# Kernel optimization log

Hardware: AMD Instinct MI355X
Metric: run time of the kernel (lower is better)

The kernel has to match this reference:

```python
import jax, jax.numpy as jnp
import numpy as np

N_DST = 25000
LEAKY = 0.2
EPS = 1e-5


def _params(dim_node=128, dim_edge=128, dim_time=100, dim_out=128):
    ks = jax.random.split(jax.random.key(1), 8)
    dq = dim_node + dim_time
    dk = dim_node + dim_edge + dim_time
    do = dim_node + dim_out
    p = {
        'w_t': jnp.asarray((1.0 / 10 ** np.linspace(0, 9, dim_time, dtype=np.float32)).reshape(dim_time, 1)),
        'b_t': jnp.zeros((dim_time,), jnp.float32),
        'Wq': jax.random.normal(ks[0], (dim_out, dq), jnp.float32) * (dq ** -0.5),
        'bq': jnp.zeros((dim_out,), jnp.float32),
        'Wk': jax.random.normal(ks[1], (dim_out, dk), jnp.float32) * (dk ** -0.5),
        'bk': jnp.zeros((dim_out,), jnp.float32),
        'Wv': jax.random.normal(ks[2], (dim_out, dk), jnp.float32) * (dk ** -0.5),
        'bv': jnp.zeros((dim_out,), jnp.float32),
        'Wout': jax.random.normal(ks[3], (dim_out, do), jnp.float32) * (do ** -0.5),
        'bout': jnp.zeros((dim_out,), jnp.float32),
        'ln_w': jnp.ones((dim_out,), jnp.float32),
        'ln_b': jnp.zeros((dim_out,), jnp.float32),
    }
    return p


def setup_inputs() -> dict:
    key = jax.random.key(0)
    k1, k2, k3, k4, k5 = jax.random.split(key, 5)
    E = 400000
    inp = {
        'h': jax.random.normal(k1, (425000, 128), jnp.float32),
        'f': jax.random.normal(k2, (E, 128), jnp.float32),
        'dt': jax.random.uniform(k3, (E,), jnp.float32) * 1e4,
        'src_idx': jax.random.randint(k4, (E,), 0, 425000, jnp.int32),
        'dst_idx': jax.random.randint(k5, (E,), 0, N_DST, jnp.int32),
    }
    inp.update(_params())
    return inp


def reference(h, f, dt, src_idx, dst_idx, w_t, b_t, Wq, bq, Wk, bk, Wv, bv, Wout, bout, ln_w, ln_b):
    num_head = 2
    dim_out = Wq.shape[0]
    E = dt.shape[0]
    # time encoding: cos(Linear(t))
    time_feat = jnp.cos(dt[:, None] * w_t[:, 0][None, :] + b_t)        # [E, dt]
    zero_time = jnp.cos(b_t)[None, :]                                   # [1, dt]
    zero_time_feat = jnp.broadcast_to(zero_time, (N_DST, b_t.shape[0]))
    # Q from dst nodes (first N_DST rows of h), gathered per edge
    q_nodes = jnp.concatenate([h[:N_DST], zero_time_feat], axis=1) @ Wq.T + bq  # [N_DST, dim_out]
    Q = q_nodes[dst_idx]                                                # [E, dim_out]
    kv_in = jnp.concatenate([h[src_idx], f, time_feat], axis=1)         # [E, dn+de+dt]
    K = kv_in @ Wk.T + bk
    V = kv_in @ Wv.T + bv
    dh = dim_out // num_head
    Qh = Q.reshape(E, num_head, dh)
    Kh = K.reshape(E, num_head, dh)
    Vh = V.reshape(E, num_head, dh)
    score = jax.nn.leaky_relu(jnp.sum(Qh * Kh, axis=2), LEAKY)          # [E, H]
    # edge softmax over incoming edges per dst node
    m = jax.ops.segment_max(score, dst_idx, num_segments=N_DST)         # [N_DST, H]
    e = jnp.exp(score - m[dst_idx])
    s = jax.ops.segment_sum(e, dst_idx, num_segments=N_DST)
    att = e / s[dst_idx]                                                # [E, H]
    Vw = (Vh * att[:, :, None]).reshape(E, dim_out)
    agg = jax.ops.segment_sum(Vw, dst_idx, num_segments=N_DST)          # [N_DST, dim_out]
    rst = jnp.concatenate([agg, h[:N_DST]], axis=1) @ Wout.T + bout
    rst = jax.nn.relu(rst)
    mu = jnp.mean(rst, axis=-1, keepdims=True)
    var = jnp.mean((rst - mu) ** 2, axis=-1, keepdims=True)
    return (rst - mu) * jax.lax.rsqrt(var + EPS) * ln_w + ln_b
```

## Files before the change

### kernel.cpp

```cpp
#include <hip/hip_runtime.h>
#include <math.h>

#define N_DST   25000
#define DN      128
#define DE      128
#define DTF     100
#define DKV     356
#define KP      384
#define DQ      228
#define DOUT    128
#define LEAKY   0.2f
#define LN_EPS  1e-5f
#define LDA     392
#define LDV     136
#define INV2PI  0.15915494309189535f

#define OFF_V       0ull
#define OFF_SCORE   102400000ull
#define OFF_QN      105600000ull
#define OFF_WS      118400000ull
#define OFF_WT      118700000ull
#define OFF_CNT     118900000ull
#define OFF_OFFS    119000000ull
#define OFF_CURSOR  119100004ull
#define OFF_ELIST   119200004ull

typedef __attribute__((ext_vector_type(8))) short short8;
typedef __attribute__((ext_vector_type(4))) float f32x4;

__device__ __forceinline__ unsigned short f2bf(float x) {
    union { float f; unsigned u; } v; v.f = x;
    unsigned r = v.u + 0x7FFFu + ((v.u >> 16) & 1u);
    return (unsigned short)(r >> 16);
}
__device__ __forceinline__ float bf2f(unsigned short u) {
    union { unsigned u; float f; } v; v.u = ((unsigned)u) << 16;
    return v.f;
}
__device__ __forceinline__ float fastcos(float x) {
    return __builtin_amdgcn_cosf(__builtin_amdgcn_fractf(x * INV2PI));
}

__global__ __launch_bounds__(128) void k_prepw(const float* __restrict__ Wk,
                                               const float* __restrict__ Wv,
                                               unsigned short* __restrict__ WS) {
    const int n = blockIdx.x;
    const float* src = (n < 128) ? &Wk[(size_t)n * DKV] : &Wv[(size_t)(n - 128) * DKV];
    const int c16 = n >> 4, t16 = n & 15;
    for (int k = threadIdx.x; k < KP; k += 128) {
        float v = (k < DKV) ? src[k] : 0.f;
        int kc = k >> 5, qd = (k >> 3) & 3, j = k & 7;
        WS[(size_t)(((kc * 16 + c16) * 64 + qd * 16 + t16) * 8 + j)] = f2bf(v);
    }
}

__global__ __launch_bounds__(128) void k_prepwt(const float* __restrict__ Wout,
                                                float* __restrict__ WT) {
    const int k = blockIdx.x;
    const int j = threadIdx.x;
    WT[k * 128 + j] = Wout[(size_t)j * 256 + k];
}

__global__ __launch_bounds__(256) void k_qnodes(const float* __restrict__ h,
                                                const float* __restrict__ Wq,
                                                const float* __restrict__ bq,
                                                const float* __restrict__ b_t,
                                                float* __restrict__ qn) {
    __shared__ float hrows[16 * 128];
    __shared__ float part[16 * 128];
    const int tid = threadIdx.x;
    const int j  = tid & 127;
    const int kh = tid >> 7;

    float wq[64];
    #pragma unroll
    for (int k = 0; k < 64; k += 4) {
        float4 w = *(const float4*)&Wq[j * DQ + kh * 64 + k];
        wq[k] = w.x; wq[k + 1] = w.y; wq[k + 2] = w.z; wq[k + 3] = w.w;
    }
    float cq = 0.f;
    if (kh == 0) {
        cq = bq[j];
        for (int k = 0; k < DTF; ++k)
            cq += Wq[j * DQ + 128 + k] * fastcos(b_t[k]);
    }

    const int r0 = blockIdx.x * 16;
    for (int u = tid; u < 512; u += 256) {
        int rr = u >> 5, q = u & 31;
        int r = r0 + rr;
        float4 v = make_float4(0.f, 0.f, 0.f, 0.f);
        if (r < N_DST) v = *(const float4*)&h[(size_t)r * DN + q * 4];
        *(float4*)&hrows[rr * 128 + q * 4] = v;
    }
    __syncthreads();

    float acc[16];
    #pragma unroll
    for (int rr = 0; rr < 16; ++rr) acc[rr] = 0.f;
    #pragma unroll
    for (int k4 = 0; k4 < 64; k4 += 4) {
        float w0 = wq[k4], w1 = wq[k4 + 1], w2 = wq[k4 + 2], w3 = wq[k4 + 3];
        #pragma unroll
        for (int rr = 0; rr < 16; ++rr) {
            float4 hv = *(float4*)&hrows[rr * 128 + kh * 64 + k4];
            acc[rr] += w0 * hv.x + w1 * hv.y + w2 * hv.z + w3 * hv.w;
        }
    }
    if (kh == 1) {
        #pragma unroll
        for (int rr = 0; rr < 16; ++rr) part[rr * 128 + j] = acc[rr];
    }
    __syncthreads();
    if (kh == 0) {
        #pragma unroll
        for (int rr = 0; rr < 16; ++rr) {
            int r = r0 + rr;
            if (r < N_DST)
                qn[(size_t)r * DOUT + j] = acc[rr] + part[rr * 128 + j] + cq;
        }
    }
}

__global__ void k_hist(const int* __restrict__ dst, int* __restrict__ cnt, int E) {
    int i = blockIdx.x * 256 + threadIdx.x;
    if (i < E) atomicAdd(&cnt[dst[i]], 1);
}

__global__ __launch_bounds__(256) void k_scan(const int* __restrict__ cnt,
                                              int* __restrict__ offs,
                                              int* __restrict__ cursor) {
    __shared__ int totals[256];
    __shared__ int bases[257];
    const int t = threadIdx.x;
    const int STRIP = (N_DST + 255) / 256;
    int s = 0;
    for (int i = 0; i < STRIP; ++i) {
        int idx = t * STRIP + i;
        if (idx < N_DST) s += cnt[idx];
    }
    totals[t] = s;
    __syncthreads();
    if (t == 0) {
        int run = 0;
        for (int i = 0; i < 256; ++i) { bases[i] = run; run += totals[i]; }
        bases[256] = run;
    }
    __syncthreads();
    int run = bases[t];
    for (int i = 0; i < STRIP; ++i) {
        int idx = t * STRIP + i;
        if (idx < N_DST) {
            offs[idx] = run;
            cursor[idx] = run;
            run += cnt[idx];
        }
    }
    if (t == 0) offs[N_DST] = bases[256];
}

__global__ void k_scatter(const int* __restrict__ dst, int* __restrict__ cursor,
                          int* __restrict__ elist, int E) {
    int i = blockIdx.x * 256 + threadIdx.x;
    if (i < E) {
        int d = dst[i];
        int pos = atomicAdd(&cursor[d], 1);
        elist[pos] = i;
    }
}

__global__ __launch_bounds__(256, 3) void k_edge(const float* __restrict__ h,
                                                 const float* __restrict__ f,
                                                 const float* __restrict__ dtv,
                                                 const int* __restrict__ src_idx,
                                                 const int* __restrict__ dst_idx,
                                                 const float* __restrict__ w_t,
                                                 const float* __restrict__ b_t,
                                                 const unsigned short* __restrict__ WS,
                                                 const float* __restrict__ bk,
                                                 const float* __restrict__ bv,
                                                 const float* __restrict__ qn,
                                                 unsigned short* __restrict__ Vout,
                                                 float* __restrict__ score,
                                                 int E) {
    __shared__ unsigned short At[64 * LDA];
    __shared__ int sidx[64];
    __shared__ int didx[64];

    const int tid = threadIdx.x;
    const int e0  = blockIdx.x * 64;

    if (tid < 64) {
        int ge = min(e0 + tid, E - 1);
        sidx[tid] = src_idx[ge];
        didx[tid] = dst_idx[ge];
    }
    __syncthreads();

    {
        const int e  = tid >> 2;
        const int qb = tid & 3;
        const int ge = min(e0 + e, E - 1);
        const int s  = sidx[e];
        const float dte = dtv[ge];
        const float* hb = &h[(size_t)s * DN];
        const float* fb = &f[(size_t)ge * DE];
        float4 buf[16];

        #pragma unroll
        for (int it = 0; it < 8; ++it) buf[it]     = *(const float4*)&hb[qb * 4 + it * 16];
        #pragma unroll
        for (int it = 0; it < 8; ++it) buf[8 + it] = *(const float4*)&fb[qb * 4 + it * 16];
        #pragma unroll
        for (int it = 0; it < 16; ++it) {
            int c = (it < 8) ? (qb * 4 + it * 16) : (128 + qb * 4 + (it - 8) * 16);
            union { unsigned short us[4]; uint2 u2; } pk;
            pk.us[0] = f2bf(buf[it].x); pk.us[1] = f2bf(buf[it].y);
            pk.us[2] = f2bf(buf[it].z); pk.us[3] = f2bf(buf[it].w);
            *(uint2*)&At[e * LDA + c] = pk.u2;
        }
        #pragma unroll
        for (int it = 0; it < 8; ++it) {
            int t0 = qb * 4 + it * 16;
            float4 v = make_float4(0.f, 0.f, 0.f, 0.f);
            if (t0 < DTF) {
                float4 wt = *(const float4*)&w_t[t0];
                float4 bt = *(const float4*)&b_t[t0];
                v.x = fastcos(dte * wt.x + bt.x);
                v.y = fastcos(dte * wt.y + bt.y);
                v.z = fastcos(dte * wt.z + bt.z);
                v.w = fastcos(dte * wt.w + bt.w);
            }
            union { unsigned short us[4]; uint2 u2; } pk;
            pk.us[0] = f2bf(v.x); pk.us[1] = f2bf(v.y);
            pk.us[2] = f2bf(v.z); pk.us[3] = f2bf(v.w);
            *(uint2*)&At[e * LDA + 256 + t0] = pk.u2;
        }
    }
    __syncthreads();

    const int lane = tid & 63;
    const int w    = tid >> 6;
    const int t16  = lane & 15;
    const int qd   = lane >> 4;
    const int w4   = w * 4;

    f32x4 acc[4][4];
    #pragma unroll
    for (int r = 0; r < 4; ++r)
        #pragma unroll
        for (int c = 0; c < 4; ++c)
            acc[r][c] = (f32x4){0.f, 0.f, 0.f, 0.f};

    short8 aC[4], aN[4], bC[4], bN[4];
    #pragma unroll
    for (int r = 0; r < 4; ++r)
        aC[r] = *(const short8*)&At[(r * 16 + t16) * LDA + qd * 8];
    #pragma unroll
    for (int c = 0; c < 4; ++c)
        bC[c] = *(const short8*)(WS + (size_t)((w4 + c) * 64 + lane) * 8);

    #pragma unroll 1
    for (int kc = 0; kc < 12; kc += 2) {
        #pragma unroll
        for (int r = 0; r < 4; ++r)
            aN[r] = *(const short8*)&At[(r * 16 + t16) * LDA + (kc + 1) * 32 + qd * 8];
        #pragma unroll
        for (int c = 0; c < 4; ++c)
            bN[c] = *(const short8*)(WS + (size_t)(((kc + 1) * 16 + w4 + c) * 64 + lane) * 8);
        #pragma unroll
        for (int r = 0; r < 4; ++r)
            #pragma unroll
            for (int c = 0; c < 4; ++c)
                acc[r][c] = __builtin_amdgcn_mfma_f32_16x16x32_bf16(aC[r], bC[c], acc[r][c], 0, 0, 0);
        if (kc + 2 < 12) {
            #pragma unroll
            for (int r = 0; r < 4; ++r)
                aC[r] = *(const short8*)&At[(r * 16 + t16) * LDA + (kc + 2) * 32 + qd * 8];
            #pragma unroll
            for (int c = 0; c < 4; ++c)
                bC[c] = *(const short8*)(WS + (size_t)(((kc + 2) * 16 + w4 + c) * 64 + lane) * 8);
        }
        #pragma unroll
        for (int r = 0; r < 4; ++r)
            #pragma unroll
            for (int c = 0; c < 4; ++c)
                acc[r][c] = __builtin_amdgcn_mfma_f32_16x16x32_bf16(aN[r], bN[c], acc[r][c], 0, 0, 0);
    }

    __syncthreads();

    if (w >= 2) {
        const int half = w - 2;
        const int vc0  = half * 64;
        float bvv[4];
        #pragma unroll
        for (int c = 0; c < 4; ++c) bvv[c] = bv[vc0 + c * 16 + t16];

        #pragma unroll
        for (int r = 0; r < 4; ++r) {
            #pragma unroll
            for (int i = 0; i < 4; ++i) {
                const int el = r * 16 + qd * 4 + i;
                #pragma unroll
                for (int c = 0; c < 4; ++c)
                    At[el * LDV + vc0 + c * 16 + t16] = f2bf(acc[r][c][i] + bvv[c]);
            }
        }
        asm volatile("s_waitcnt lgkmcnt(0)" ::: "memory");

        const int row0 = lane >> 3;
        const int ch   = lane & 7;
        #pragma unroll
        for (int it = 0; it < 8; ++it) {
            const int el = row0 + it * 8;
            const int ge = e0 + el;
            short8 vv = *(const short8*)&At[el * LDV + vc0 + ch * 8];
            if (ge < E)
                *(short8*)&Vout[(size_t)ge * DOUT + vc0 + ch * 8] = vv;
        }
    } else {
        float bkc[4];
        #pragma unroll
        for (int c = 0; c < 4; ++c)
            bkc[c] = bk[w * 64 + c * 16 + t16];
        #pragma unroll
        for (int r = 0; r < 4; ++r) {
            float qv[4][4];
            #pragma unroll
            for (int i = 0; i < 4; ++i) {
                const int d = didx[r * 16 + qd * 4 + i];
                const float* qrow = &qn[(size_t)d * DOUT + w * 64 + t16];
                qv[i][0] = qrow[0];
                qv[i][1] = qrow[16];
                qv[i][2] = qrow[32];
                qv[i][3] = qrow[48];
            }
            #pragma unroll
            for (int i = 0; i < 4; ++i) {
                float p = (acc[r][0][i] + bkc[0]) * qv[i][0]
                        + (acc[r][1][i] + bkc[1]) * qv[i][1]
                        + (acc[r][2][i] + bkc[2]) * qv[i][2]
                        + (acc[r][3][i] + bkc[3]) * qv[i][3];
                p += __shfl_xor(p, 1);
                p += __shfl_xor(p, 2);
                p += __shfl_xor(p, 4);
                p += __shfl_xor(p, 8);
                if (t16 == 0) {
                    const int ge = e0 + r * 16 + qd * 4 + i;
                    if (ge < E) {
                        float sc = (p >= 0.f) ? p : LEAKY * p;
                        score[(size_t)ge * 2 + w] = sc;
                    }
                }
            }
        }
    }
}

__global__ __launch_bounds__(512) void k_dst(const unsigned short* __restrict__ V,
                                             const float* __restrict__ score,
                                             const int* __restrict__ offs,
                                             const int* __restrict__ elist,
                                             const float* __restrict__ h,
                                             const float* __restrict__ WT,
                                             const float* __restrict__ bout,
                                             const float* __restrict__ ln_w,
                                             const float* __restrict__ ln_b,
                                             float* __restrict__ out) {
    const int tid = threadIdx.x;
    const int s   = tid >> 5;
    const int t32 = tid & 31;
    const int d   = blockIdx.x * 16 + s;
    const bool valid = d < N_DST;
    const int beg = valid ? offs[d] : 0;
    const int end = valid ? offs[d + 1] : 0;

    __shared__ float inc[16][256];
    __shared__ float wchunk[64 * 128];

    float m0 = -1e30f, m1 = -1e30f;
    for (int i = beg + t32; i < end; i += 32) {
        int e = elist[i];
        float2 sc = *(const float2*)&score[(size_t)e * 2];
        m0 = fmaxf(m0, sc.x);
        m1 = fmaxf(m1, sc.y);
    }
    #pragma unroll
    for (int o = 1; o < 32; o <<= 1) {
        m0 = fmaxf(m0, __shfl_xor(m0, o));
        m1 = fmaxf(m1, __shfl_xor(m1, o));
    }
    const int   hd = t32 >> 4;
    const float mh = hd ? m1 : m0;

    float a0 = 0.f, a1 = 0.f, a2 = 0.f, a3 = 0.f, l = 0.f;
    int i = beg;
    for (; i + 1 < end; i += 2) {
        int ea = elist[i], eb = elist[i + 1];
        float s0 = score[(size_t)ea * 2 + hd];
        float s1 = score[(size_t)eb * 2 + hd];
        ushort4 v0 = *(const ushort4*)&V[(size_t)ea * DOUT + t32 * 4];
        ushort4 v1 = *(const ushort4*)&V[(size_t)eb * DOUT + t32 * 4];
        float w0 = __expf(s0 - mh);
        float w1 = __expf(s1 - mh);
        l += w0 + w1;
        a0 += w0 * bf2f(v0.x) + w1 * bf2f(v1.x);
        a1 += w0 * bf2f(v0.y) + w1 * bf2f(v1.y);
        a2 += w0 * bf2f(v0.z) + w1 * bf2f(v1.z);
        a3 += w0 * bf2f(v0.w) + w1 * bf2f(v1.w);
    }
    if (i < end) {
        int ea = elist[i];
        float s0 = score[(size_t)ea * 2 + hd];
        ushort4 v0 = *(const ushort4*)&V[(size_t)ea * DOUT + t32 * 4];
        float w0 = __expf(s0 - mh);
        l += w0;
        a0 += w0 * bf2f(v0.x);
        a1 += w0 * bf2f(v0.y);
        a2 += w0 * bf2f(v0.z);
        a3 += w0 * bf2f(v0.w);
    }
    float inv = (l > 0.f) ? (1.f / l) : 0.f;
    inc[s][t32 * 4 + 0] = a0 * inv;
    inc[s][t32 * 4 + 1] = a1 * inv;
    inc[s][t32 * 4 + 2] = a2 * inv;
    inc[s][t32 * 4 + 3] = a3 * inv;
    {
        float4 hh = make_float4(0.f, 0.f, 0.f, 0.f);
        if (valid) hh = *(const float4*)&h[(size_t)d * DN + t32 * 4];
        *(float4*)&inc[s][128 + t32 * 4] = hh;
    }

    float4 r4 = *(const float4*)&bout[t32 * 4];
    #pragma unroll 1
    for (int ch = 0; ch < 4; ++ch) {
        __syncthreads();
        for (int u = tid; u < 2048; u += 512)
            *(float4*)&wchunk[u * 4] = *(const float4*)&WT[(size_t)ch * 8192 + u * 4];
        __syncthreads();
        #pragma unroll 4
        for (int kk = 0; kk < 64; ++kk) {
            float ic = inc[s][ch * 64 + kk];
            float4 w4 = *(float4*)&wchunk[kk * 128 + t32 * 4];
            r4.x += w4.x * ic;
            r4.y += w4.y * ic;
            r4.z += w4.z * ic;
            r4.w += w4.w * ic;
        }
    }
    r4.x = fmaxf(r4.x, 0.f);
    r4.y = fmaxf(r4.y, 0.f);
    r4.z = fmaxf(r4.z, 0.f);
    r4.w = fmaxf(r4.w, 0.f);

    float s1 = r4.x + r4.y + r4.z + r4.w;
    float s2 = r4.x * r4.x + r4.y * r4.y + r4.z * r4.z + r4.w * r4.w;
    #pragma unroll
    for (int o = 1; o < 32; o <<= 1) {
        s1 += __shfl_xor(s1, o);
        s2 += __shfl_xor(s2, o);
    }
    float mu  = s1 * (1.f / 128.f);
    float var = s2 * (1.f / 128.f) - mu * mu;
    float rsd = rsqrtf(var + LN_EPS);
    if (valid) {
        float4 lw = *(const float4*)&ln_w[t32 * 4];
        float4 lb = *(const float4*)&ln_b[t32 * 4];
        float4 o4;
        o4.x = (r4.x - mu) * rsd * lw.x + lb.x;
        o4.y = (r4.y - mu) * rsd * lw.y + lb.y;
        o4.z = (r4.z - mu) * rsd * lw.z + lb.z;
        o4.w = (r4.w - mu) * rsd * lw.w + lb.w;
        *(float4*)&out[(size_t)d * DOUT + t32 * 4] = o4;
    }
}

extern "C" void kernel_launch(void* const* d_in, const int* in_sizes, int n_in,
                              void* d_out, int out_size, void* d_ws, size_t ws_size,
                              hipStream_t stream) {
    const float* h       = (const float*)d_in[0];
    const float* f       = (const float*)d_in[1];
    const float* dt      = (const float*)d_in[2];
    const int*   src_idx = (const int*)d_in[3];
    const int*   dst_idx = (const int*)d_in[4];
    const float* w_t     = (const float*)d_in[5];
    const float* b_t     = (const float*)d_in[6];
    const float* Wq      = (const float*)d_in[7];
    const float* bq      = (const float*)d_in[8];
    const float* Wk      = (const float*)d_in[9];
    const float* bk      = (const float*)d_in[10];
    const float* Wv      = (const float*)d_in[11];
    const float* bv      = (const float*)d_in[12];
    const float* Wout    = (const float*)d_in[13];
    const float* bout    = (const float*)d_in[14];
    const float* ln_w    = (const float*)d_in[15];
    const float* ln_b    = (const float*)d_in[16];
    float*       out     = (float*)d_out;

    const int E = in_sizes[2];

    char* ws = (char*)d_ws;
    unsigned short* V  = (unsigned short*)(ws + OFF_V);
    float* score       = (float*)(ws + OFF_SCORE);
    float* qn          = (float*)(ws + OFF_QN);
    unsigned short* WS = (unsigned short*)(ws + OFF_WS);
    float* WT          = (float*)(ws + OFF_WT);
    int*   cnt         = (int*)(ws + OFF_CNT);
    int*   offs        = (int*)(ws + OFF_OFFS);
    int*   cursor      = (int*)(ws + OFF_CURSOR);
    int*   elist       = (int*)(ws + OFF_ELIST);

    hipMemsetAsync(cnt, 0, N_DST * sizeof(int), stream);

    k_prepw<<<256, 128, 0, stream>>>(Wk, Wv, WS);
    k_prepwt<<<256, 128, 0, stream>>>(Wout, WT);
    k_qnodes<<<(N_DST + 15) / 16, 256, 0, stream>>>(h, Wq, bq, b_t, qn);
    k_hist<<<(E + 255) / 256, 256, 0, stream>>>(dst_idx, cnt, E);
    k_scan<<<1, 256, 0, stream>>>(cnt, offs, cursor);
    k_scatter<<<(E + 255) / 256, 256, 0, stream>>>(dst_idx, cursor, elist, E);
    k_edge<<<(E + 63) / 64, 256, 0, stream>>>(h, f, dt, src_idx, dst_idx,
                                              w_t, b_t, WS, bk, bv, qn, V, score, E);
    k_dst<<<(N_DST + 15) / 16, 512, 0, stream>>>(V, score, offs, elist, h, WT, bout,
                                                 ln_w, ln_b, out);
}
```

Baseline: 770.9 us.

## Shrink edge tile to 48 and stage K dimension in two swizzled LDS halves

The edge kernel now handles 48 edges per block instead of 64. The 384-wide bf16 input tile is staged in two 192-column halves in a smaller XOR-swizzled LDS buffer, which cuts LDS use and registers. The launch bound rises to 4 blocks per SM to raise occupancy, and the swizzle is meant to avoid bank conflicts. In exchange it adds an extra barrier phase, drops the explicit A/B register double-buffering, and launches more blocks that each reuse the weights less.

```diff
diff --git a/kernel.cpp b/kernel.cpp
--- a/kernel.cpp
+++ b/kernel.cpp
@@ -11,7 +11,7 @@
 #define DOUT    128
 #define LEAKY   0.2f
 #define LN_EPS  1e-5f
-#define LDA     392
+#define EB      48
 #define LDV     136
 #define INV2PI  0.15915494309189535f
 
@@ -169,7 +169,7 @@
     }
 }
 
-__global__ __launch_bounds__(256, 3) void k_edge(const float* __restrict__ h,
+__global__ __launch_bounds__(256, 4) void k_edge(const float* __restrict__ h,
                                                  const float* __restrict__ f,
                                                  const float* __restrict__ dtv,
                                                  const int* __restrict__ src_idx,
@@ -183,59 +183,19 @@
                                                  unsigned short* __restrict__ Vout,
                                                  float* __restrict__ score,
                                                  int E) {
-    __shared__ unsigned short At[64 * LDA];
-    __shared__ int sidx[64];
-    __shared__ int didx[64];
+    __shared__ unsigned short At[EB * 192];
+    __shared__ int   sidx[EB];
+    __shared__ int   didx[EB];
+    __shared__ float sdt[EB];
 
     const int tid = threadIdx.x;
-    const int e0  = blockIdx.x * 64;
-
-    if (tid < 64) {
+    const int e0  = blockIdx.x * EB;
+
+    if (tid < EB) {
         int ge = min(e0 + tid, E - 1);
         sidx[tid] = src_idx[ge];
         didx[tid] = dst_idx[ge];
-    }
-    __syncthreads();
-
-    {
-        const int e  = tid >> 2;
-        const int qb = tid & 3;
-        const int ge = min(e0 + e, E - 1);
-        const int s  = sidx[e];
-        const float dte = dtv[ge];
-        const float* hb = &h[(size_t)s * DN];
-        const float* fb = &f[(size_t)ge * DE];
-        float4 buf[16];
-
-        #pragma unroll
-        for (int it = 0; it < 8; ++it) buf[it]     = *(const float4*)&hb[qb * 4 + it * 16];
-        #pragma unroll
-        for (int it = 0; it < 8; ++it) buf[8 + it] = *(const float4*)&fb[qb * 4 + it * 16];
-        #pragma unroll
-        for (int it = 0; it < 16; ++it) {
-            int c = (it < 8) ? (qb * 4 + it * 16) : (128 + qb * 4 + (it - 8) * 16);
-            union { unsigned short us[4]; uint2 u2; } pk;
-            pk.us[0] = f2bf(buf[it].x); pk.us[1] = f2bf(buf[it].y);
-            pk.us[2] = f2bf(buf[it].z); pk.us[3] = f2bf(buf[it].w);
-            *(uint2*)&At[e * LDA + c] = pk.u2;
-        }
-        #pragma unroll
-        for (int it = 0; it < 8; ++it) {
-            int t0 = qb * 4 + it * 16;
-            float4 v = make_float4(0.f, 0.f, 0.f, 0.f);
-            if (t0 < DTF) {
-                float4 wt = *(const float4*)&w_t[t0];
-                float4 bt = *(const float4*)&b_t[t0];
-                v.x = fastcos(dte * wt.x + bt.x);
-                v.y = fastcos(dte * wt.y + bt.y);
-                v.z = fastcos(dte * wt.z + bt.z);
-                v.w = fastcos(dte * wt.w + bt.w);
-            }
-            union { unsigned short us[4]; uint2 u2; } pk;
-            pk.us[0] = f2bf(v.x); pk.us[1] = f2bf(v.y);
-            pk.us[2] = f2bf(v.z); pk.us[3] = f2bf(v.w);
-            *(uint2*)&At[e * LDA + 256 + t0] = pk.u2;
-        }
+        sdt[tid]  = dtv[ge];
     }
     __syncthreads();
 
@@ -245,50 +205,68 @@
     const int qd   = lane >> 4;
     const int w4   = w * 4;
 
-    f32x4 acc[4][4];
-    #pragma unroll
-    for (int r = 0; r < 4; ++r)
+    f32x4 acc[3][4];
+    #pragma unroll
+    for (int r = 0; r < 3; ++r)
         #pragma unroll
         for (int c = 0; c < 4; ++c)
             acc[r][c] = (f32x4){0.f, 0.f, 0.f, 0.f};
 
-    short8 aC[4], aN[4], bC[4], bN[4];
-    #pragma unroll
-    for (int r = 0; r < 4; ++r)
-        aC[r] = *(const short8*)&At[(r * 16 + t16) * LDA + qd * 8];
-    #pragma unroll
-    for (int c = 0; c < 4; ++c)
-        bC[c] = *(const short8*)(WS + (size_t)((w4 + c) * 64 + lane) * 8);
-
-    #pragma unroll 1
-    for (int kc = 0; kc < 12; kc += 2) {
-        #pragma unroll
-        for (int r = 0; r < 4; ++r)
-            aN[r] = *(const short8*)&At[(r * 16 + t16) * LDA + (kc + 1) * 32 + qd * 8];
-        #pragma unroll
-        for (int c = 0; c < 4; ++c)
-            bN[c] = *(const short8*)(WS + (size_t)(((kc + 1) * 16 + w4 + c) * 64 + lane) * 8);
-        #pragma unroll
-        for (int r = 0; r < 4; ++r)
+    #pragma unroll
+    for (int p = 0; p < 2; ++p) {
+        #pragma unroll
+        for (int k = 0; k < 5; ++k) {
+            int u = tid + k * 256;
+            if (u < EB * 24) {
+                int e  = u / 24;
+                int j  = u - e * 24;
+                int c0 = p * 192 + j * 8;
+                int ge = min(e0 + e, E - 1);
+                float v[8];
+                if (c0 < 256) {
+                    const float* src = (c0 < 128)
+                        ? &h[(size_t)sidx[e] * DN + c0]
+                        : &f[(size_t)ge * DE + (c0 - 128)];
+                    float4 x = *(const float4*)src;
+                    float4 y = *(const float4*)(src + 4);
+                    v[0] = x.x; v[1] = x.y; v[2] = x.z; v[3] = x.w;
+                    v[4] = y.x; v[5] = y.y; v[6] = y.z; v[7] = y.w;
+                } else {
+                    const float dte = sdt[e];
+                    const int t0 = c0 - 256;
+                    #pragma unroll
+                    for (int i2 = 0; i2 < 8; ++i2) {
+                        int c = t0 + i2;
+                        v[i2] = (c < DTF) ? fastcos(dte * w_t[c] + b_t[c]) : 0.f;
+                    }
+                }
+                short8 pk;
+                #pragma unroll
+                for (int i2 = 0; i2 < 8; ++i2) pk[i2] = (short)f2bf(v[i2]);
+                *(short8*)&At[(unsigned)((e * 192 + j * 8) ^ ((e & 7) << 3))] = pk;
+            }
+        }
+        __syncthreads();
+
+        #pragma unroll
+        for (int kcl = 0; kcl < 6; ++kcl) {
+            const int kg = p * 6 + kcl;
+            short8 a[3], b[4];
+            #pragma unroll
+            for (int r = 0; r < 3; ++r)
+                a[r] = *(const short8*)&At[(unsigned)(
+                    (((r * 16 + t16) * 192) + kcl * 32 + qd * 8) ^ ((t16 & 7) << 3))];
             #pragma unroll
             for (int c = 0; c < 4; ++c)
-                acc[r][c] = __builtin_amdgcn_mfma_f32_16x16x32_bf16(aC[r], bC[c], acc[r][c], 0, 0, 0);
-        if (kc + 2 < 12) {
+                b[c] = *(const short8*)(WS + (size_t)((kg * 16 + w4 + c) * 64 + lane) * 8);
             #pragma unroll
-            for (int r = 0; r < 4; ++r)
-                aC[r] = *(const short8*)&At[(r * 16 + t16) * LDA + (kc + 2) * 32 + qd * 8];
-            #pragma unroll
-            for (int c = 0; c < 4; ++c)
-                bC[c] = *(const short8*)(WS + (size_t)(((kc + 2) * 16 + w4 + c) * 64 + lane) * 8);
-        }
-        #pragma unroll
-        for (int r = 0; r < 4; ++r)
-            #pragma unroll
-            for (int c = 0; c < 4; ++c)
-                acc[r][c] = __builtin_amdgcn_mfma_f32_16x16x32_bf16(aN[r], bN[c], acc[r][c], 0, 0, 0);
-    }
-
-    __syncthreads();
+            for (int r = 0; r < 3; ++r)
+                #pragma unroll
+                for (int c = 0; c < 4; ++c)
+                    acc[r][c] = __builtin_amdgcn_mfma_f32_16x16x32_bf16(a[r], b[c], acc[r][c], 0, 0, 0);
+        }
+        __syncthreads();
+    }
 
     if (w >= 2) {
         const int half = w - 2;
@@ -298,7 +276,7 @@
         for (int c = 0; c < 4; ++c) bvv[c] = bv[vc0 + c * 16 + t16];
 
         #pragma unroll
-        for (int r = 0; r < 4; ++r) {
+        for (int r = 0; r < 3; ++r) {
             #pragma unroll
             for (int i = 0; i < 4; ++i) {
                 const int el = r * 16 + qd * 4 + i;
@@ -312,7 +290,7 @@
         const int row0 = lane >> 3;
         const int ch   = lane & 7;
         #pragma unroll
-        for (int it = 0; it < 8; ++it) {
+        for (int it = 0; it < 6; ++it) {
             const int el = row0 + it * 8;
             const int ge = e0 + el;
             short8 vv = *(const short8*)&At[el * LDV + vc0 + ch * 8];
@@ -325,7 +303,7 @@
         for (int c = 0; c < 4; ++c)
             bkc[c] = bk[w * 64 + c * 16 + t16];
         #pragma unroll
-        for (int r = 0; r < 4; ++r) {
+        for (int r = 0; r < 3; ++r) {
             float qv[4][4];
             #pragma unroll
             for (int i = 0; i < 4; ++i) {
@@ -519,8 +497,8 @@
     k_hist<<<(E + 255) / 256, 256, 0, stream>>>(dst_idx, cnt, E);
     k_scan<<<1, 256, 0, stream>>>(cnt, offs, cursor);
     k_scatter<<<(E + 255) / 256, 256, 0, stream>>>(dst_idx, cursor, elist, E);
-    k_edge<<<(E + 63) / 64, 256, 0, stream>>>(h, f, dt, src_idx, dst_idx,
-                                              w_t, b_t, WS, bk, bv, qn, V, score, E);
+    k_edge<<<(E + EB - 1) / EB, 256, 0, stream>>>(h, f, dt, src_idx, dst_idx,
+                                                  w_t, b_t, WS, bk, bv, qn, V, score, E);
     k_dst<<<(N_DST + 15) / 16, 512, 0, stream>>>(V, score, offs, elist, h, WT, bout,
                                                  ln_w, ln_b, out);
 }
```

Result: slower. 946.4 us (+22.8%).

## Write edge V and scores in dst-sorted order to remove elist indirection

Applied to the files above, without the earlier changes.

The scatter kernel now records each edge's position in the dst-sorted order instead of building an edge list. The edge kernel writes V rows and scores directly to those sorted positions, so the destination kernel reads contiguous V and scores without a dependent elist load. The destination loop is unrolled by four, and the Wq time-bias loop in k_qnodes is vectorised. In exchange, the edge kernel now does scattered writes instead of coalesced ones.

```diff
diff --git a/kernel.cpp b/kernel.cpp
--- a/kernel.cpp
+++ b/kernel.cpp
@@ -23,7 +23,7 @@
 #define OFF_CNT     118900000ull
 #define OFF_OFFS    119000000ull
 #define OFF_CURSOR  119100004ull
-#define OFF_ELIST   119200004ull
+#define OFF_EPOS    119200004ull
 
 typedef __attribute__((ext_vector_type(8))) short short8;
 typedef __attribute__((ext_vector_type(4))) float f32x4;
@@ -81,8 +81,13 @@
     float cq = 0.f;
     if (kh == 0) {
         cq = bq[j];
-        for (int k = 0; k < DTF; ++k)
-            cq += Wq[j * DQ + 128 + k] * fastcos(b_t[k]);
+        #pragma unroll
+        for (int k = 0; k < DTF; k += 4) {
+            float4 wv = *(const float4*)&Wq[j * DQ + 128 + k];
+            float4 bt = *(const float4*)&b_t[k];
+            cq += wv.x * fastcos(bt.x) + wv.y * fastcos(bt.y)
+                + wv.z * fastcos(bt.z) + wv.w * fastcos(bt.w);
+        }
     }
 
     const int r0 = blockIdx.x * 16;
@@ -160,12 +165,11 @@
 }
 
 __global__ void k_scatter(const int* __restrict__ dst, int* __restrict__ cursor,
-                          int* __restrict__ elist, int E) {
+                          int* __restrict__ epos, int E) {
     int i = blockIdx.x * 256 + threadIdx.x;
     if (i < E) {
         int d = dst[i];
-        int pos = atomicAdd(&cursor[d], 1);
-        elist[pos] = i;
+        epos[i] = atomicAdd(&cursor[d], 1);
     }
 }
 
@@ -174,6 +178,7 @@
                                                  const float* __restrict__ dtv,
                                                  const int* __restrict__ src_idx,
                                                  const int* __restrict__ dst_idx,
+                                                 const int* __restrict__ epos,
                                                  const float* __restrict__ w_t,
                                                  const float* __restrict__ b_t,
                                                  const unsigned short* __restrict__ WS,
@@ -186,6 +191,7 @@
     __shared__ unsigned short At[64 * LDA];
     __shared__ int sidx[64];
     __shared__ int didx[64];
+    __shared__ int spos[64];
 
     const int tid = threadIdx.x;
     const int e0  = blockIdx.x * 64;
@@ -194,6 +200,7 @@
         int ge = min(e0 + tid, E - 1);
         sidx[tid] = src_idx[ge];
         didx[tid] = dst_idx[ge];
+        spos[tid] = epos[ge];
     }
     __syncthreads();
 
@@ -317,7 +324,7 @@
             const int ge = e0 + el;
             short8 vv = *(const short8*)&At[el * LDV + vc0 + ch * 8];
             if (ge < E)
-                *(short8*)&Vout[(size_t)ge * DOUT + vc0 + ch * 8] = vv;
+                *(short8*)&Vout[(size_t)spos[el] * DOUT + vc0 + ch * 8] = vv;
         }
     } else {
         float bkc[4];
@@ -347,10 +354,11 @@
                 p += __shfl_xor(p, 4);
                 p += __shfl_xor(p, 8);
                 if (t16 == 0) {
-                    const int ge = e0 + r * 16 + qd * 4 + i;
+                    const int el = r * 16 + qd * 4 + i;
+                    const int ge = e0 + el;
                     if (ge < E) {
                         float sc = (p >= 0.f) ? p : LEAKY * p;
-                        score[(size_t)ge * 2 + w] = sc;
+                        score[(size_t)spos[el] * 2 + w] = sc;
                     }
                 }
             }
@@ -361,7 +369,6 @@
 __global__ __launch_bounds__(512) void k_dst(const unsigned short* __restrict__ V,
                                              const float* __restrict__ score,
                                              const int* __restrict__ offs,
-                                             const int* __restrict__ elist,
                                              const float* __restrict__ h,
                                              const float* __restrict__ WT,
                                              const float* __restrict__ bout,
@@ -381,8 +388,7 @@
 
     float m0 = -1e30f, m1 = -1e30f;
     for (int i = beg + t32; i < end; i += 32) {
-        int e = elist[i];
-        float2 sc = *(const float2*)&score[(size_t)e * 2];
+        float2 sc = *(const float2*)&score[(size_t)i * 2];
         m0 = fmaxf(m0, sc.x);
         m1 = fmaxf(m1, sc.y);
     }
@@ -396,24 +402,28 @@
 
     float a0 = 0.f, a1 = 0.f, a2 = 0.f, a3 = 0.f, l = 0.f;
     int i = beg;
-    for (; i + 1 < end; i += 2) {
-        int ea = elist[i], eb = elist[i + 1];
-        float s0 = score[(size_t)ea * 2 + hd];
-        float s1 = score[(size_t)eb * 2 + hd];
-        ushort4 v0 = *(const ushort4*)&V[(size_t)ea * DOUT + t32 * 4];
-        ushort4 v1 = *(const ushort4*)&V[(size_t)eb * DOUT + t32 * 4];
+    for (; i + 3 < end; i += 4) {
+        float s0 = score[(size_t)(i + 0) * 2 + hd];
+        float s1 = score[(size_t)(i + 1) * 2 + hd];
+        float s2 = score[(size_t)(i + 2) * 2 + hd];
+        float s3 = score[(size_t)(i + 3) * 2 + hd];
+        ushort4 v0 = *(const ushort4*)&V[(size_t)(i + 0) * DOUT + t32 * 4];
+        ushort4 v1 = *(const ushort4*)&V[(size_t)(i + 1) * DOUT + t32 * 4];
+        ushort4 v2 = *(const ushort4*)&V[(size_t)(i + 2) * DOUT + t32 * 4];
+        ushort4 v3 = *(const ushort4*)&V[(size_t)(i + 3) * DOUT + t32 * 4];
         float w0 = __expf(s0 - mh);
         float w1 = __expf(s1 - mh);
-        l += w0 + w1;
-        a0 += w0 * bf2f(v0.x) + w1 * bf2f(v1.x);
-        a1 += w0 * bf2f(v0.y) + w1 * bf2f(v1.y);
-        a2 += w0 * bf2f(v0.z) + w1 * bf2f(v1.z);
-        a3 += w0 * bf2f(v0.w) + w1 * bf2f(v1.w);
-    }
-    if (i < end) {
-        int ea = elist[i];
-        float s0 = score[(size_t)ea * 2 + hd];
-        ushort4 v0 = *(const ushort4*)&V[(size_t)ea * DOUT + t32 * 4];
+        float w2 = __expf(s2 - mh);
+        float w3 = __expf(s3 - mh);
+        l += (w0 + w1) + (w2 + w3);
+        a0 += w0 * bf2f(v0.x) + w1 * bf2f(v1.x) + w2 * bf2f(v2.x) + w3 * bf2f(v3.x);
+        a1 += w0 * bf2f(v0.y) + w1 * bf2f(v1.y) + w2 * bf2f(v2.y) + w3 * bf2f(v3.y);
+        a2 += w0 * bf2f(v0.z) + w1 * bf2f(v1.z) + w2 * bf2f(v2.z) + w3 * bf2f(v3.z);
+        a3 += w0 * bf2f(v0.w) + w1 * bf2f(v1.w) + w2 * bf2f(v2.w) + w3 * bf2f(v3.w);
+    }
+    for (; i < end; ++i) {
+        float s0 = score[(size_t)i * 2 + hd];
+        ushort4 v0 = *(const ushort4*)&V[(size_t)i * DOUT + t32 * 4];
         float w0 = __expf(s0 - mh);
         l += w0;
         a0 += w0 * bf2f(v0.x);
@@ -509,7 +519,7 @@
     int*   cnt         = (int*)(ws + OFF_CNT);
     int*   offs        = (int*)(ws + OFF_OFFS);
     int*   cursor      = (int*)(ws + OFF_CURSOR);
-    int*   elist       = (int*)(ws + OFF_ELIST);
+    int*   epos        = (int*)(ws + OFF_EPOS);
 
     hipMemsetAsync(cnt, 0, N_DST * sizeof(int), stream);
 
@@ -518,9 +528,9 @@
     k_qnodes<<<(N_DST + 15) / 16, 256, 0, stream>>>(h, Wq, bq, b_t, qn);
     k_hist<<<(E + 255) / 256, 256, 0, stream>>>(dst_idx, cnt, E);
     k_scan<<<1, 256, 0, stream>>>(cnt, offs, cursor);
-    k_scatter<<<(E + 255) / 256, 256, 0, stream>>>(dst_idx, cursor, elist, E);
-    k_edge<<<(E + 63) / 64, 256, 0, stream>>>(h, f, dt, src_idx, dst_idx,
+    k_scatter<<<(E + 255) / 256, 256, 0, stream>>>(dst_idx, cursor, epos, E);
+    k_edge<<<(E + 63) / 64, 256, 0, stream>>>(h, f, dt, src_idx, dst_idx, epos,
                                               w_t, b_t, WS, bk, bv, qn, V, score, E);
-    k_dst<<<(N_DST + 15) / 16, 512, 0, stream>>>(V, score, offs, elist, h, WT, bout,
+    k_dst<<<(N_DST + 15) / 16, 512, 0, stream>>>(V, score, offs, h, WT, bout,
                                                  ln_w, ln_b, out);
 }
```

Measured after the change: 738.1 us. 4.3% less time.
